# Performance work log

Measured on AMD Instinct MI355X. Metric: run time of the kernel, lower is better.

Reference implementation:

```python
import jax, jax.numpy as jnp
import numpy as np
from jax import lax

K = 3  # kernel_size
PAD = 1
STRIDE = 1
DIL = 1


def setup_inputs() -> dict:
    key = jax.random.key(0)
    k1, k2 = jax.random.split(key)
    x = jax.random.normal(k1, (32, 256, 56, 56), dtype=jnp.float32)
    weights = jax.random.normal(k2, (256, 256, K * K), dtype=jnp.float32) * 0.05
    return {"x": x, "weights": weights}


def reference(x, weights):
    B, C, H, W = x.shape
    O = weights.shape[0]
    # weights stored as [O, C, k*k] -> standard OIHW conv kernel
    w = weights.reshape(O, C, K, K)
    # Dense conv replaces the per-(channel, filter) matmul loop over im2col windows.
    y = lax.conv_general_dilated(
        x, w,
        window_strides=(STRIDE, STRIDE),
        padding=[(PAD, PAD), (PAD, PAD)],
        rhs_dilation=(DIL, DIL),
        dimension_numbers=("NCHW", "OIHW", "NCHW"),
    )  # [B, O, Hout, Wout]
    Hout, Wout = y.shape[2], y.shape[3]
    # Faithful to original: results buffer is laid out [O, B, Hout, Wout]
    # (out-channel-major blocks of batch) then reinterpreted as [B, O, Hout, Wout].
    result = jnp.transpose(y, (1, 0, 2, 3)).reshape(B, O, Hout, Wout)
    return result
```

## Files before the change

### kernel.cpp

```cpp
#include <hip/hip_runtime.h>
#include <hip/hip_bf16.h>

using s8v   = __attribute__((ext_vector_type(8))) short;
using f32x4 = __attribute__((ext_vector_type(4))) float;

#define N_TOT 100352
#define WT_ELEMS 589824
#define PLANE_ELEMS 861184
#define XT_ELEMS 27557888
#define WS_NEED  56295424

__device__ __forceinline__ unsigned short f2bf(float f) {
    unsigned int u = __float_as_uint(f);
    unsigned int r = (u + 0x7FFF + ((u >> 16) & 1)) >> 16;
    return (unsigned short)r;
}

__device__ __forceinline__ void gl_lds16(const void* g, void* l) {
    __builtin_amdgcn_global_load_lds(
        (const __attribute__((address_space(1))) unsigned int*)g,
        (__attribute__((address_space(3))) unsigned int*)l, 16, 0, 0);
}

__global__ void prep_w(const float* __restrict__ w, unsigned short* __restrict__ wt) {
    int u = blockIdx.x * 256 + threadIdx.x;
    int kt = u >> 11;
    int r  = u & 2047;
    int o  = r >> 3;
    int s  = r & 7;
    int ksub  = s ^ (o & 7);
    int kstep = kt * 2 + (ksub >> 2);
    int cb = kstep / 9, tap = kstep - cb * 9;
    int c0 = cb * 32 + (ksub & 3) * 8;
    const float* src = w + ((size_t)(o * 256 + c0)) * 9 + tap;
    unsigned int p[4];
    #pragma unroll
    for (int q = 0; q < 4; ++q) {
        float f0 = src[(2 * q) * 9];
        float f1 = src[(2 * q + 1) * 9];
        p[q] = (unsigned)f2bf(f0) | ((unsigned)f2bf(f1) << 16);
    }
    *(uint4*)(wt + (size_t)u * 8) = *(uint4*)p;
}

__global__ void prep_x(const float* __restrict__ x, unsigned short* __restrict__ xt) {
    int b  = blockIdx.x / 58;
    int hp = blockIdx.x % 58;
    int tid = threadIdx.x;
    uint4 zero = {0u, 0u, 0u, 0u};
    size_t rowbase = (size_t)(b * 58 + hp) * 58;
    if (hp == 0 || hp == 57) {
        for (int i = tid; i < 1856; i += 256) {
            int cg = i / 58, wp = i - cg * 58;
            *(uint4*)(xt + ((size_t)cg * PLANE_ELEMS + (rowbase + wp) * 8)) = zero;
        }
        return;
    }
    int h = hp - 1;
    int wave = tid >> 6, lane = tid & 63;
    for (int cg = wave; cg < 32; cg += 4) {
        unsigned short* outp = xt + (size_t)cg * PLANE_ELEMS + rowbase * 8;
        if (lane < 56) {
            const float* src = x + ((size_t)(b * 256 + cg * 8) * 3136 + h * 56 + lane);
            unsigned int p[4];
            #pragma unroll
            for (int q = 0; q < 4; ++q) {
                float f0 = src[(size_t)(2 * q) * 3136];
                float f1 = src[(size_t)(2 * q + 1) * 3136];
                p[q] = (unsigned)f2bf(f0) | ((unsigned)f2bf(f1) << 16);
            }
            *(uint4*)(outp + (size_t)(lane + 1) * 8) = *(uint4*)p;
        } else if (lane == 56) {
            *(uint4*)outp = zero;
        } else if (lane == 57) {
            *(uint4*)(outp + 57 * 8) = zero;
        }
    }
}

__global__ __launch_bounds__(512, 2) void gemm8(const unsigned short* __restrict__ wt,
                                                const unsigned short* __restrict__ xt,
                                                float* __restrict__ out) {
    extern __shared__ char lds[];
    int bx = blockIdx.x;
    int nt = (bx & 7) * 49 + (bx >> 3);
    int tid  = threadIdx.x;
    int w    = tid >> 6, lane = tid & 63;
    int l16  = lane & 15, quad = lane >> 4;
    int wm   = w >> 2,   wn   = w & 3;

    int ksub  = (lane & 7) ^ (lane >> 3);
    int ksl   = ksub >> 2;
    int c2off = (ksub & 3) * PLANE_ELEMS;
    int pixoff[4];
    #pragma unroll
    for (int it = 0; it < 4; ++it) {
        int n = nt * 256 + w * 32 + it * 8 + (lane >> 3);
        int b = n / 3136; int rr = n - b * 3136;
        int h = rr / 56;  int ww = rr - h * 56;
        pixoff[it] = ((b * 58 + h) * 58 + ww) * 8;
    }

    int swz = (quad ^ (l16 & 7)) << 4;
    int aK0 = wm * 16384 + l16 * 128 + swz;
    int aK1 = aK0 ^ 64;
    int bK0 = 32768 + wn * 8192 + l16 * 128 + swz;
    int bK1 = bK0 ^ 64;

    auto STAGE = [&](char* buf, const unsigned short* aP, int bo0, int bo1) {
        #pragma unroll
        for (int it = 0; it < 4; ++it)
            gl_lds16(aP + it * 4096 + w * 512 + lane * 8, buf + it * 8192 + w * 1024);
        int bsel = (ksl ? bo1 : bo0) + c2off;
        #pragma unroll
        for (int it = 0; it < 4; ++it)
            gl_lds16(xt + (size_t)(unsigned)(bsel + pixoff[it]),
                     buf + 32768 + w * 4096 + it * 1024);
    };

    f32x4 acc[8][4] = {};

    STAGE(lds, wt, 0, 1 * 8);
    const unsigned short* aP = wt + 16384;

    #pragma unroll 2
    for (int t = 0; t < 36; ++t) {
        if (t < 35) {
            int kk  = 2 * (t + 1);
            int cb0 = kk / 9,       tap0 = kk - cb0 * 9;
            int cb1 = (kk + 1) / 9, tap1 = (kk + 1) - cb1 * 9;
            int ts0 = (tap0 / 3) * 58 + tap0 - (tap0 / 3) * 3;
            int ts1 = (tap1 / 3) * 58 + tap1 - (tap1 / 3) * 3;
            STAGE(lds + ((t + 1) & 1) * 65536, aP,
                  cb0 * 4 * PLANE_ELEMS + ts0 * 8,
                  cb1 * 4 * PLANE_ELEMS + ts1 * 8);
            aP += 16384;
            asm volatile("s_waitcnt vmcnt(8)" ::: "memory");
        } else {
            asm volatile("s_waitcnt vmcnt(0)" ::: "memory");
        }
        asm volatile("s_barrier" ::: "memory");
        const char* base = lds + (t & 1) * 65536;
        #pragma unroll
        for (int mh = 0; mh < 2; ++mh) {
            s8v af0[4], af1[4];
            #pragma unroll
            for (int f = 0; f < 4; ++f) {
                af0[f] = *(const s8v*)(base + aK0 + (mh * 4 + f) * 2048);
                af1[f] = *(const s8v*)(base + aK1 + (mh * 4 + f) * 2048);
            }
            #pragma unroll
            for (int nh = 0; nh < 2; ++nh) {
                s8v bf0[2], bf1[2];
                #pragma unroll
                for (int g = 0; g < 2; ++g) {
                    bf0[g] = *(const s8v*)(base + bK0 + (nh * 2 + g) * 2048);
                    bf1[g] = *(const s8v*)(base + bK1 + (nh * 2 + g) * 2048);
                }
                __builtin_amdgcn_s_setprio(1);
                #pragma unroll
                for (int f = 0; f < 4; ++f)
                    #pragma unroll
                    for (int g = 0; g < 2; ++g) {
                        f32x4 c = acc[mh * 4 + f][nh * 2 + g];
                        c = __builtin_amdgcn_mfma_f32_16x16x32_bf16(af0[f], bf0[g], c, 0, 0, 0);
                        c = __builtin_amdgcn_mfma_f32_16x16x32_bf16(af1[f], bf1[g], c, 0, 0, 0);
                        acc[mh * 4 + f][nh * 2 + g] = c;
                    }
                __builtin_amdgcn_s_setprio(0);
            }
        }
        asm volatile("s_barrier" ::: "memory");
    }

    float* op = out + (size_t)(wm * 128 + quad * 4) * N_TOT + nt * 256 + wn * 64 + l16;
    #pragma unroll
    for (int f = 0; f < 8; ++f)
        #pragma unroll
        for (int rr = 0; rr < 4; ++rr) {
            float* orow = op + (size_t)(f * 16 + rr) * N_TOT;
            #pragma unroll
            for (int g = 0; g < 4; ++g)
                orow[g * 16] = acc[f][g][rr];
        }
}

__global__ void conv_naive(const float* __restrict__ x, const float* __restrict__ wq,
                           float* __restrict__ out) {
    int f = blockIdx.x * 256 + threadIdx.x;
    int o = f / N_TOT;
    int n = f - o * N_TOT;
    int b = n / 3136; int r = n - b * 3136; int h = r / 56; int w = r - h * 56;
    const float* xb = x + (size_t)b * 256 * 3136;
    const float* wo = wq + o * 2304;
    float acc = 0.f;
    for (int c = 0; c < 256; ++c) {
        const float* xc = xb + c * 3136;
        const float* wc = wo + c * 9;
        #pragma unroll
        for (int dh = 0; dh < 3; ++dh) {
            int ih = h + dh - 1;
            if (ih < 0 || ih >= 56) continue;
            const float* xr = xc + ih * 56;
            #pragma unroll
            for (int dw = 0; dw < 3; ++dw) {
                int iw = w + dw - 1;
                if (iw >= 0 && iw < 56) acc += xr[iw] * wc[dh * 3 + dw];
            }
        }
    }
    out[f] = acc;
}

extern "C" void kernel_launch(void* const* d_in, const int* in_sizes, int n_in,
                              void* d_out, int out_size, void* d_ws, size_t ws_size,
                              hipStream_t stream) {
    const float* x = (const float*)d_in[0];
    const float* w = (const float*)d_in[1];
    float* out = (float*)d_out;
    if (ws_size >= (size_t)WS_NEED) {
        unsigned short* wt = (unsigned short*)d_ws;
        unsigned short* xt = wt + WT_ELEMS;
        static int attr_done = 0;
        if (!attr_done) {
            hipFuncSetAttribute((const void*)gemm8,
                                hipFuncAttributeMaxDynamicSharedMemorySize, 131072);
            attr_done = 1;
        }
        prep_w<<<288, 256, 0, stream>>>(w, wt);
        prep_x<<<32 * 58, 256, 0, stream>>>(x, xt);
        gemm8<<<392, 512, 131072, stream>>>(wt, xt, out);
    } else {
        conv_naive<<<N_TOT, 256, 0, stream>>>(x, w, out);
    }
}
```

Baseline: 341.0 us.

## Restructure GEMM main loop into four-phase interleaved load/compute pipeline

Splits each K-step of the bf16 MFMA conv GEMM into four phases, one per quarter of the output tile. Global-to-LDS loads for future stages are issued between phases, with some written into the current buffer once its fragments are consumed, so the pipeline runs two steps ahead. Fragment reads are reorganised so A and B fragments are reused across phases. The aim is better overlap of memory traffic with MFMA work and shallower vmcnt stalls, at the cost of many more barriers per iteration and tighter ordering of buffer reuse.

New measurement: 328.7 us. 1.04x faster.

```diff
diff --git a/kernel.cpp b/kernel.cpp
--- a/kernel.cpp
+++ b/kernel.cpp
@@ -9,6 +9,8 @@
 #define PLANE_ELEMS 861184
 #define XT_ELEMS 27557888
 #define WS_NEED  56295424
+
+#define BAR() asm volatile("s_barrier" ::: "memory")
 
 __device__ __forceinline__ unsigned short f2bf(float f) {
     unsigned int u = __float_as_uint(f);
@@ -88,18 +90,29 @@
     int w    = tid >> 6, lane = tid & 63;
     int l16  = lane & 15, quad = lane >> 4;
     int wm   = w >> 2,   wn   = w & 3;
-
+    int lane16 = lane * 16;
+
+    int s0 = w * 2, s1 = w * 2 + 1;
+    int adst0 = ((s0 >> 3) * 128 + (s0 & 7) * 8) * 128;
+    int adst1 = ((s1 >> 3) * 128 + (s1 & 7) * 8) * 128;
+    int bp0 = ((s0 >> 2) * 64 + (s0 & 3) * 8);
+    int bp1 = ((s1 >> 2) * 64 + (s1 & 3) * 8);
+    int bdst0 = bp0 * 128;
+    int bdst1 = bp1 * 128;
     int ksub  = (lane & 7) ^ (lane >> 3);
     int ksl   = ksub >> 2;
     int c2off = (ksub & 3) * PLANE_ELEMS;
-    int pixoff[4];
+    int pix[2][2];
     #pragma unroll
-    for (int it = 0; it < 4; ++it) {
-        int n = nt * 256 + w * 32 + it * 8 + (lane >> 3);
-        int b = n / 3136; int rr = n - b * 3136;
-        int h = rr / 56;  int ww = rr - h * 56;
-        pixoff[it] = ((b * 58 + h) * 58 + ww) * 8;
-    }
+    for (int it = 0; it < 2; ++it)
+        #pragma unroll
+        for (int h = 0; h < 2; ++h) {
+            int n = nt * 256 + (it ? bp1 : bp0) + h * 32 + (lane >> 3);
+            int b = n / 3136; int rr = n - b * 3136;
+            int hh = rr / 56; int ww = rr - hh * 56;
+            pix[it][h] = ((b * 58 + hh) * 58 + ww) * 8;
+        }
+    int pix00 = pix[0][0], pix01 = pix[0][1], pix10 = pix[1][0], pix11 = pix[1][1];
 
     int swz = (quad ^ (l16 & 7)) << 4;
     int aK0 = wm * 16384 + l16 * 128 + swz;
@@ -107,70 +120,103 @@
     int bK0 = 32768 + wn * 8192 + l16 * 128 + swz;
     int bK1 = bK0 ^ 64;
 
-    auto STAGE = [&](char* buf, const unsigned short* aP, int bo0, int bo1) {
-        #pragma unroll
-        for (int it = 0; it < 4; ++it)
-            gl_lds16(aP + it * 4096 + w * 512 + lane * 8, buf + it * 8192 + w * 1024);
+    auto SA = [&](char* buf, const char* srcTile, int roff) {
+        gl_lds16(srcTile + adst0 + roff + lane16, buf + adst0 + roff);
+        gl_lds16(srcTile + adst1 + roff + lane16, buf + adst1 + roff);
+    };
+    auto SB = [&](char* buf, int bo0, int bo1, int h) {
         int bsel = (ksl ? bo1 : bo0) + c2off;
-        #pragma unroll
-        for (int it = 0; it < 4; ++it)
-            gl_lds16(xt + (size_t)(unsigned)(bsel + pixoff[it]),
-                     buf + 32768 + w * 4096 + it * 1024);
+        gl_lds16(xt + (size_t)(unsigned)(bsel + (h ? pix01 : pix00)),
+                 buf + 32768 + bdst0 + h * 4096);
+        gl_lds16(xt + (size_t)(unsigned)(bsel + (h ? pix11 : pix10)),
+                 buf + 32768 + bdst1 + h * 4096);
     };
+    auto BO = [&](int ks) {
+        int cb = ks / 9, tap = ks - cb * 9;
+        return cb * 4 * PLANE_ELEMS + ((tap / 3) * 58 + (tap - (tap / 3) * 3)) * 8;
+    };
 
     f32x4 acc[8][4] = {};
-
-    STAGE(lds, wt, 0, 1 * 8);
-    const unsigned short* aP = wt + 16384;
-
-    #pragma unroll 2
+    s8v a0[4], a1[4], b00[2], b01[2], b10[2], b11[2];
+
+    SA(lds, (const char*)wt, 0);
+    SA(lds, (const char*)wt, 8192);
+    SB(lds, BO(0), BO(1), 0);
+    SB(lds, BO(0), BO(1), 1);
+    SA(lds + 65536, (const char*)wt + 32768, 0);
+    SB(lds + 65536, BO(2), BO(3), 0);
+    SB(lds + 65536, BO(2), BO(3), 1);
+    asm volatile("s_waitcnt vmcnt(6)" ::: "memory");
+    BAR();
+
+    #define PHASE_MFMA(MH, NH, BA, BB)                                             \
+        __builtin_amdgcn_s_setprio(1);                                             \
+        _Pragma("unroll")                                                          \
+        for (int f = 0; f < 4; ++f) {                                              \
+            _Pragma("unroll")                                                      \
+            for (int g = 0; g < 2; ++g) {                                          \
+                f32x4 c = acc[(MH)*4 + f][(NH)*2 + g];                             \
+                c = __builtin_amdgcn_mfma_f32_16x16x32_bf16(a0[f], BA[g], c, 0, 0, 0); \
+                c = __builtin_amdgcn_mfma_f32_16x16x32_bf16(a1[f], BB[g], c, 0, 0, 0); \
+                acc[(MH)*4 + f][(NH)*2 + g] = c;                                   \
+            }                                                                      \
+        }                                                                          \
+        __builtin_amdgcn_s_setprio(0);
+
+    #pragma unroll 1
     for (int t = 0; t < 36; ++t) {
-        if (t < 35) {
-            int kk  = 2 * (t + 1);
-            int cb0 = kk / 9,       tap0 = kk - cb0 * 9;
-            int cb1 = (kk + 1) / 9, tap1 = (kk + 1) - cb1 * 9;
-            int ts0 = (tap0 / 3) * 58 + tap0 - (tap0 / 3) * 3;
-            int ts1 = (tap1 / 3) * 58 + tap1 - (tap1 / 3) * 3;
-            STAGE(lds + ((t + 1) & 1) * 65536, aP,
-                  cb0 * 4 * PLANE_ELEMS + ts0 * 8,
-                  cb1 * 4 * PLANE_ELEMS + ts1 * 8);
-            aP += 16384;
-            asm volatile("s_waitcnt vmcnt(8)" ::: "memory");
-        } else {
+        char* bufc = lds + (t & 1) * 65536;
+        char* bufo = lds + ((t & 1) ^ 1) * 65536;
+        const char* wA1 = (const char*)wt + (size_t)(t + 1) * 32768;
+        const char* wA0 = (const char*)wt + (size_t)(t + 2) * 32768;
+        int kk  = 2 * (t + 2);
+        int bo0 = BO(kk);
+        int bo1 = BO(kk + 1);
+
+        #pragma unroll
+        for (int f = 0; f < 4; ++f) {
+            a0[f] = *(const s8v*)(bufc + aK0 + f * 2048);
+            a1[f] = *(const s8v*)(bufc + aK1 + f * 2048);
+        }
+        #pragma unroll
+        for (int g = 0; g < 2; ++g) {
+            b00[g] = *(const s8v*)(bufc + bK0 + g * 2048);
+            b01[g] = *(const s8v*)(bufc + bK1 + g * 2048);
+        }
+        if (t < 35) SA(bufo, wA1, 8192);
+        BAR();
+        PHASE_MFMA(0, 0, b00, b01)
+        BAR();
+
+        #pragma unroll
+        for (int g = 0; g < 2; ++g) {
+            b10[g] = *(const s8v*)(bufc + bK0 + 4096 + g * 2048);
+            b11[g] = *(const s8v*)(bufc + bK1 + 4096 + g * 2048);
+        }
+        if (t < 34) SA(bufc, wA0, 0);
+        BAR();
+        PHASE_MFMA(0, 1, b10, b11)
+        BAR();
+
+        #pragma unroll
+        for (int f = 0; f < 4; ++f) {
+            a0[f] = *(const s8v*)(bufc + aK0 + 8192 + f * 2048);
+            a1[f] = *(const s8v*)(bufc + aK1 + 8192 + f * 2048);
+        }
+        if (t < 34) SB(bufc, bo0, bo1, 0);
+        BAR();
+        PHASE_MFMA(1, 0, b00, b01)
+        BAR();
+
+        if (t < 34) {
+            SB(bufc, bo0, bo1, 1);
+            asm volatile("s_waitcnt vmcnt(6)" ::: "memory");
+        } else if (t == 34) {
             asm volatile("s_waitcnt vmcnt(0)" ::: "memory");
         }
-        asm volatile("s_barrier" ::: "memory");
-        const char* base = lds + (t & 1) * 65536;
-        #pragma unroll
-        for (int mh = 0; mh < 2; ++mh) {
-            s8v af0[4], af1[4];
-            #pragma unroll
-            for (int f = 0; f < 4; ++f) {
-                af0[f] = *(const s8v*)(base + aK0 + (mh * 4 + f) * 2048);
-                af1[f] = *(const s8v*)(base + aK1 + (mh * 4 + f) * 2048);
-            }
-            #pragma unroll
-            for (int nh = 0; nh < 2; ++nh) {
-                s8v bf0[2], bf1[2];
-                #pragma unroll
-                for (int g = 0; g < 2; ++g) {
-                    bf0[g] = *(const s8v*)(base + bK0 + (nh * 2 + g) * 2048);
-                    bf1[g] = *(const s8v*)(base + bK1 + (nh * 2 + g) * 2048);
-                }
-                __builtin_amdgcn_s_setprio(1);
-                #pragma unroll
-                for (int f = 0; f < 4; ++f)
-                    #pragma unroll
-                    for (int g = 0; g < 2; ++g) {
-                        f32x4 c = acc[mh * 4 + f][nh * 2 + g];
-                        c = __builtin_amdgcn_mfma_f32_16x16x32_bf16(af0[f], bf0[g], c, 0, 0, 0);
-                        c = __builtin_amdgcn_mfma_f32_16x16x32_bf16(af1[f], bf1[g], c, 0, 0, 0);
-                        acc[mh * 4 + f][nh * 2 + g] = c;
-                    }
-                __builtin_amdgcn_s_setprio(0);
-            }
-        }
-        asm volatile("s_barrier" ::: "memory");
+        BAR();
+        PHASE_MFMA(1, 1, b10, b11)
+        BAR();
     }
 
     float* op = out + (size_t)(wm * 128 + quad * 4) * N_TOT + nt * 256 + wn * 64 + l16;
```
